# Kernel optimization log

Hardware: AMD Instinct MI355X
Metric: run time of the kernel (lower is better)

## Reference

```python
import jax, jax.numpy as jnp
import numpy as np

D_MODEL, N_LAYER, VOCAB = 166, 3, 26
D_INNER, D_STATE, D_CONV, DT_RANK = 332, 16, 4, 11
EPS = 1e-5


def setup_inputs() -> dict:
    key = jax.random.key(0)
    ks = jax.random.split(key, 12)
    B, L = 16, 1024
    n = lambda k, s, sc=0.05: jax.random.normal(k, s, jnp.float32) * sc
    # mamba-style dt bias init: softplus(bias) ~ U[1e-3, 0.1]
    dt_init = jax.random.uniform(ks[7], (N_LAYER, D_INNER), jnp.float32, 1e-3, 0.1)
    return {
        "fasta": jax.random.randint(ks[0], (B, L), 0, VOCAB),
        "embed": n(ks[1], (VOCAB, D_MODEL), 0.02),
        "in_proj_w": n(ks[2], (N_LAYER, 2 * D_INNER, D_MODEL)),
        "conv_w": n(ks[3], (N_LAYER, D_INNER, D_CONV), 0.2),
        "conv_b": n(ks[4], (N_LAYER, D_INNER), 0.02),
        "x_proj_w": n(ks[5], (N_LAYER, DT_RANK + 2 * D_STATE, D_INNER)),
        "dt_proj_w": n(ks[6], (N_LAYER, D_INNER, DT_RANK), 0.1),
        "dt_proj_b": jnp.log(jnp.expm1(dt_init)),
        "A_log": jnp.log(jnp.tile(jnp.arange(1, D_STATE + 1, dtype=jnp.float32), (N_LAYER, D_INNER, 1))),
        "D": jnp.ones((N_LAYER, D_INNER), jnp.float32),
        "out_proj_w": n(ks[8], (N_LAYER, D_MODEL, D_INNER)),
        "norm_w": jnp.ones((N_LAYER, D_MODEL), jnp.float32),
        "norm_f_w": jnp.ones((D_MODEL,), jnp.float32),
    }


def rmsnorm(x, w):
    return x * jax.lax.rsqrt(jnp.mean(x * x, axis=-1, keepdims=True) + EPS) * w


def mamba_layer(h, in_w, cw, cb, xw, dtw, dtb, A_log, Dp, ow):
    b, L, _ = h.shape
    xz = h @ in_w.T                              # (b, L, 2*d_inner)
    x, z = jnp.split(xz, 2, axis=-1)
    # causal depthwise conv1d, kernel D_CONV
    xp = jnp.pad(x, ((0, 0), (D_CONV - 1, 0), (0, 0)))
    x = sum(xp[:, j:j + L, :] * cw[:, j] for j in range(D_CONV)) + cb
    x = jax.nn.silu(x)                           # u: (b, L, d_inner)
    dbc = x @ xw.T                               # (b, L, dt_rank + 2*d_state)
    dt = dbc[..., :DT_RANK]
    Bm = dbc[..., DT_RANK:DT_RANK + D_STATE]
    Cm = dbc[..., DT_RANK + D_STATE:]
    dt = jax.nn.softplus(dt @ dtw.T + dtb)       # (b, L, d_inner)
    A = -jnp.exp(A_log)                          # (d_inner, d_state)
    # time-major selective scan
    ins = (jnp.moveaxis(dt, 1, 0), jnp.moveaxis(x, 1, 0),
           jnp.moveaxis(Bm, 1, 0), jnp.moveaxis(Cm, 1, 0))

    def step(hst, t):
        dt_i, x_i, B_i, C_i = t                  # (b,d) (b,d) (b,n) (b,n)
        dA = jnp.exp(dt_i[..., None] * A)        # (b, d, n)
        hst = dA * hst + (dt_i * x_i)[..., None] * B_i[:, None, :]
        y = jnp.einsum('bdn,bn->bd', hst, C_i)
        return hst, y

    h0 = jnp.zeros((b, D_INNER, D_STATE), x.dtype)
    _, ys = jax.lax.scan(step, h0, ins)
    y = jnp.moveaxis(ys, 0, 1) + Dp * x          # (b, L, d_inner)
    y = y * jax.nn.silu(z)
    return y @ ow.T                              # (b, L, d_model)


def reference(fasta, embed, in_proj_w, conv_w, conv_b, x_proj_w, dt_proj_w,
              dt_proj_b, A_log, D, out_proj_w, norm_w, norm_f_w):
    hidden = embed[fasta]                        # (b, L, d_model)
    residual = None
    for l in range(N_LAYER):
        residual = hidden if residual is None else hidden + residual
        hidden = rmsnorm(residual, norm_w[l])
        hidden = mamba_layer(hidden, in_proj_w[l], conv_w[l], conv_b[l],
                             x_proj_w[l], dt_proj_w[l], dt_proj_b[l],
                             A_log[l], D[l], out_proj_w[l])
    residual = hidden + residual
    v = rmsnorm(residual, norm_f_w)              # (b, L, d_model)
    ve = jnp.max(v, axis=1)                      # (b, d_model)
    return (ve, v)
```

## Files before the change

kernel.cpp:

```cpp
#include <hip/hip_runtime.h>
#include <math.h>

#define D_MODEL 166
#define N_LAYER 3
#define D_INNER 332
#define D_STATE 16
#define D_CONV  4
#define DT_RANK 11
#define BATCH   16
#define SEQ     1024
#define EPS     1e-5f
#define DBC_W   (DT_RANK + 2 * D_STATE)

#define CH 64
#define CL 16

#define KP_IN  192
#define KP_X   352

typedef unsigned short u16;
typedef __attribute__((ext_vector_type(8))) short short8;
typedef __attribute__((ext_vector_type(8))) unsigned short ushort8;
typedef __attribute__((ext_vector_type(4))) float f32x4;

__device__ inline u16 f2bf(float f) {
    unsigned int u = __float_as_uint(f);
    u += 0x7fff + ((u >> 16) & 1);
    return (u16)(u >> 16);
}
__device__ inline float bf2f(u16 u) {
    return __uint_as_float(((unsigned int)u) << 16);
}

__device__ inline void dt_step(float a, float& dtv, float& p) {
    if (a > 15.f) {
        dtv = a;
        p = __expf(-a);
    } else {
        float e = __expf(a);
        dtv = __logf(1.f + e);
        p = 1.f / (1.f + e);
    }
}

#define T1C (N_LAYER * 704 * KP_IN)
#define T2C (N_LAYER * 64 * KP_X)
#define T3C (N_LAYER * 192 * KP_X)
#define NB_CVT ((T1C + T2C + T3C + 255) / 256)
__global__ void k_prep(const int* __restrict__ fasta, const float* __restrict__ embed,
                       const float* __restrict__ w1, const float* __restrict__ w2,
                       const float* __restrict__ w3, const float* __restrict__ nw,
                       float* __restrict__ res, u16* __restrict__ o1,
                       u16* __restrict__ o2, u16* __restrict__ o3) {
    int blk = blockIdx.x;
    if (blk < BATCH * SEQ) {
        int m = threadIdx.x;
        if (m < D_MODEL)
            res[(size_t)blk * D_MODEL + m] = embed[(size_t)fasta[blk] * D_MODEL + m];
        return;
    }
    int idx = (blk - BATCH * SEQ) * 256 + threadIdx.x;
    if (idx < T1C) {
        int per = 704 * KP_IN;
        int l = idx / per, rr = idx - l * per;
        int n = rr / KP_IN, k = rr - n * KP_IN;
        float v = (n < 2 * D_INNER && k < D_MODEL)
                      ? w1[((size_t)l * 2 * D_INNER + n) * D_MODEL + k] * nw[l * D_MODEL + k]
                      : 0.f;
        o1[idx] = f2bf(v);
    } else if (idx < T1C + T2C) {
        int r = idx - T1C;
        int per = 64 * KP_X;
        int l = r / per, rr = r - l * per;
        int n = rr / KP_X, k = rr - n * KP_X;
        float v = (n < DBC_W && k < D_INNER) ? w2[((size_t)l * DBC_W + n) * D_INNER + k] : 0.f;
        o2[r] = f2bf(v);
    } else if (idx < T1C + T2C + T3C) {
        int r = idx - T1C - T2C;
        int per = 192 * KP_X;
        int l = r / per, rr = r - l * per;
        int n = rr / KP_X, k = rr - n * KP_X;
        float v = (n < D_MODEL && k < D_INNER) ? w3[((size_t)l * D_MODEL + n) * D_INNER + k] : 0.f;
        o3[r] = f2bf(v);
    }
}

__global__ __launch_bounds__(256) void k_gemm_in(const float* __restrict__ res,
                                                 const u16* __restrict__ Wbf,
                                                 u16* __restrict__ xb,
                                                 u16* __restrict__ zb) {
    __shared__ __align__(16) u16 As[128 * 40];
    __shared__ __align__(16) u16 Bs[64 * 40];
    __shared__ float sScale[128];
    int id = blockIdx.x;
    {
        int q = (int)gridDim.x >> 3;
        id = (id & 7) * q + (id >> 3);
    }
    int my = id / 11;
    int m0 = my * 128;
    int n0 = (id - my * 11) * 64;
    int t = threadIdx.x;
    int lr = t & 15, lk = (t >> 4) & 3;
    int wid = t >> 6, wr = wid & 1, wc = wid >> 1;
    int arow = t >> 2, ach = t & 3;

    f32x4 acc[4][2];
#pragma unroll
    for (int i = 0; i < 4; i++)
#pragma unroll
        for (int j = 0; j < 2; j++) acc[i][j] = (f32x4){0.f, 0.f, 0.f, 0.f};

    float ssq0 = 0.f, ssq1 = 0.f;
    for (int k0 = 0; k0 < KP_IN; k0 += 32) {
        int c0 = k0 + ach * 8;
#pragma unroll
        for (int half = 0; half < 2; half++) {
            int row = m0 + arow + half * 64;
            const float* rp = res + (size_t)row * D_MODEL;
            float v[8];
            if (c0 + 8 <= D_MODEL) {
#pragma unroll
                for (int j = 0; j < 4; j++) {
                    float2 f2 = *(const float2*)&rp[c0 + j * 2];
                    v[j * 2] = f2.x; v[j * 2 + 1] = f2.y;
                }
            } else {
#pragma unroll
                for (int j = 0; j < 8; j++) v[j] = (c0 + j < D_MODEL) ? rp[c0 + j] : 0.f;
            }
            float s = 0.f;
            ushort8 st;
#pragma unroll
            for (int j = 0; j < 8; j++) { s += v[j] * v[j]; st[j] = f2bf(v[j]); }
            if (half == 0) ssq0 += s; else ssq1 += s;
            *(ushort8*)&As[(arow + half * 64) * 40 + ach * 8] = st;
        }
        *(ushort8*)&Bs[arow * 40 + ach * 8] =
            *(const ushort8*)&Wbf[(size_t)(n0 + arow) * KP_IN + k0 + ach * 8];
        __syncthreads();
        short8 a[4], b[2];
#pragma unroll
        for (int mi = 0; mi < 4; mi++)
            a[mi] = *(const short8*)&As[(wr * 64 + mi * 16 + lr) * 40 + lk * 8];
#pragma unroll
        for (int ni = 0; ni < 2; ni++)
            b[ni] = *(const short8*)&Bs[(wc * 32 + ni * 16 + lr) * 40 + lk * 8];
#pragma unroll
        for (int mi = 0; mi < 4; mi++)
#pragma unroll
            for (int ni = 0; ni < 2; ni++)
                acc[mi][ni] = __builtin_amdgcn_mfma_f32_16x16x32_bf16(
                    a[mi], b[ni], acc[mi][ni], 0, 0, 0);
        __syncthreads();
    }
    ssq0 += __shfl_xor(ssq0, 1); ssq0 += __shfl_xor(ssq0, 2);
    ssq1 += __shfl_xor(ssq1, 1); ssq1 += __shfl_xor(ssq1, 2);
    if (ach == 0) {
        sScale[arow] = rsqrtf(ssq0 / (float)D_MODEL + EPS);
        sScale[arow + 64] = rsqrtf(ssq1 / (float)D_MODEL + EPS);
    }
    __syncthreads();

#pragma unroll
    for (int mi = 0; mi < 4; mi++) {
#pragma unroll
        for (int ni = 0; ni < 2; ni++) {
#pragma unroll
            for (int i = 0; i < 4; i++) {
                int rl = wr * 64 + mi * 16 + lk * 4 + i;
                int row = m0 + rl;
                int col = n0 + wc * 32 + ni * 16 + lr;
                float v = acc[mi][ni][i] * sScale[rl];
                if (col < D_INNER)
                    xb[(size_t)row * D_INNER + col] = f2bf(v);
                else if (col < 2 * D_INNER)
                    zb[(size_t)row * D_INNER + col - D_INNER] = f2bf(v);
            }
        }
    }
}

__global__ void k_conv(const u16* __restrict__ xb, const float* __restrict__ cw,
                       const float* __restrict__ cb, u16* __restrict__ xcb) {
    int bl = blockIdx.x;
    int pd = threadIdx.x;
    int d = pd * 2;
    unsigned int* outp = (unsigned int*)(xcb + (size_t)bl * KP_X);
    if (d < D_INNER) {
        int l = bl & (SEQ - 1);
        const unsigned int* p = (const unsigned int*)(xb + (size_t)bl * D_INNER) + pd;
        unsigned int v3 = p[0];
        unsigned int v2 = (l >= 1) ? p[-(D_INNER / 2)] : 0u;
        unsigned int v1 = (l >= 2) ? p[-2 * (D_INNER / 2)] : 0u;
        unsigned int v0 = (l >= 3) ? p[-3 * (D_INNER / 2)] : 0u;
        float4 wA = *(const float4*)&cw[d * 4];
        float4 wB = *(const float4*)&cw[(d + 1) * 4];
        float sa = cb[d]     + bf2f((u16)v0) * wA.x + bf2f((u16)v1) * wA.y +
                   bf2f((u16)v2) * wA.z + bf2f((u16)v3) * wA.w;
        float sb = cb[d + 1] + bf2f((u16)(v0 >> 16)) * wB.x + bf2f((u16)(v1 >> 16)) * wB.y +
                   bf2f((u16)(v2 >> 16)) * wB.z + bf2f((u16)(v3 >> 16)) * wB.w;
        float ra = sa / (1.f + __expf(-sa));
        float rb = sb / (1.f + __expf(-sb));
        outp[pd] = (unsigned int)f2bf(ra) | ((unsigned int)f2bf(rb) << 16);
    } else if (d < KP_X) {
        outp[pd] = 0u;
    }
}

__global__ __launch_bounds__(256) void k_gemm_x(const u16* __restrict__ Abf,
                                                const u16* __restrict__ Wbf,
                                                float* __restrict__ dbc) {
    __shared__ __align__(16) u16 As[64 * 40];
    __shared__ __align__(16) u16 Bs[64 * 40];
    int m0 = blockIdx.x * 64;
    int t = threadIdx.x;
    int lr = t & 15, lk = (t >> 4) & 3;
    int wid = t >> 6, wr = wid & 1, wc = wid >> 1;
    int arow = t >> 2, ach = t & 3;

    f32x4 acc[2][2];
#pragma unroll
    for (int i = 0; i < 2; i++)
#pragma unroll
        for (int j = 0; j < 2; j++) acc[i][j] = (f32x4){0.f, 0.f, 0.f, 0.f};

    for (int k0 = 0; k0 < KP_X; k0 += 32) {
        *(ushort8*)&As[arow * 40 + ach * 8] =
            *(const ushort8*)&Abf[(size_t)(m0 + arow) * KP_X + k0 + ach * 8];
        *(ushort8*)&Bs[arow * 40 + ach * 8] =
            *(const ushort8*)&Wbf[(size_t)arow * KP_X + k0 + ach * 8];
        __syncthreads();
        short8 a[2], b[2];
#pragma unroll
        for (int mi = 0; mi < 2; mi++)
            a[mi] = *(const short8*)&As[(wr * 32 + mi * 16 + lr) * 40 + lk * 8];
#pragma unroll
        for (int ni = 0; ni < 2; ni++)
            b[ni] = *(const short8*)&Bs[(wc * 32 + ni * 16 + lr) * 40 + lk * 8];
#pragma unroll
        for (int mi = 0; mi < 2; mi++)
#pragma unroll
            for (int ni = 0; ni < 2; ni++)
                acc[mi][ni] = __builtin_amdgcn_mfma_f32_16x16x32_bf16(
                    a[mi], b[ni], acc[mi][ni], 0, 0, 0);
        __syncthreads();
    }
#pragma unroll
    for (int mi = 0; mi < 2; mi++) {
#pragma unroll
        for (int ni = 0; ni < 2; ni++) {
#pragma unroll
            for (int i = 0; i < 4; i++) {
                int row = m0 + wr * 32 + mi * 16 + lk * 4 + i;
                int col = wc * 32 + ni * 16 + lr;
                if (col < DBC_W)
                    dbc[(size_t)row * DBC_W + col] = acc[mi][ni][i];
            }
        }
    }
}

__global__ __launch_bounds__(256) void k_gemm_out(const u16* __restrict__ Abf,
                                                  const u16* __restrict__ Wbf,
                                                  float* __restrict__ C) {
    __shared__ __align__(16) u16 As[128 * 40];
    __shared__ __align__(16) u16 Bs[64 * 40];
    int id = blockIdx.x;
    {
        int q = (int)gridDim.x >> 3;
        id = (id & 7) * q + (id >> 3);
    }
    int my = id / 3;
    int m0 = my * 128;
    int n0 = (id - my * 3) * 64;
    int t = threadIdx.x;
    int lr = t & 15, lk = (t >> 4) & 3;
    int wid = t >> 6, wr = wid & 1, wc = wid >> 1;
    int arow = t >> 2, ach = t & 3;

    f32x4 acc[4][2];
#pragma unroll
    for (int i = 0; i < 4; i++)
#pragma unroll
        for (int j = 0; j < 2; j++) acc[i][j] = (f32x4){0.f, 0.f, 0.f, 0.f};

    for (int k0 = 0; k0 < KP_X; k0 += 32) {
        *(ushort8*)&As[arow * 40 + ach * 8] =
            *(const ushort8*)&Abf[(size_t)(m0 + arow) * KP_X + k0 + ach * 8];
        *(ushort8*)&As[(arow + 64) * 40 + ach * 8] =
            *(const ushort8*)&Abf[(size_t)(m0 + arow + 64) * KP_X + k0 + ach * 8];
        *(ushort8*)&Bs[arow * 40 + ach * 8] =
            *(const ushort8*)&Wbf[(size_t)(n0 + arow) * KP_X + k0 + ach * 8];
        __syncthreads();
        short8 a[4], b[2];
#pragma unroll
        for (int mi = 0; mi < 4; mi++)
            a[mi] = *(const short8*)&As[(wr * 64 + mi * 16 + lr) * 40 + lk * 8];
#pragma unroll
        for (int ni = 0; ni < 2; ni++)
            b[ni] = *(const short8*)&Bs[(wc * 32 + ni * 16 + lr) * 40 + lk * 8];
#pragma unroll
        for (int mi = 0; mi < 4; mi++)
#pragma unroll
            for (int ni = 0; ni < 2; ni++)
                acc[mi][ni] = __builtin_amdgcn_mfma_f32_16x16x32_bf16(
                    a[mi], b[ni], acc[mi][ni], 0, 0, 0);
        __syncthreads();
    }
#pragma unroll
    for (int mi = 0; mi < 4; mi++) {
#pragma unroll
        for (int ni = 0; ni < 2; ni++) {
#pragma unroll
            for (int i = 0; i < 4; i++) {
                int row = m0 + wr * 64 + mi * 16 + lk * 4 + i;
                int col = n0 + wc * 32 + ni * 16 + lr;
                if (col < D_MODEL)
                    C[(size_t)row * D_MODEL + col] += acc[mi][ni][i];
            }
        }
    }
}

__global__ void k_scan1(const u16* __restrict__ xcb, const float* __restrict__ dbc,
                        const float* __restrict__ dtw, const float* __restrict__ dtb,
                        u16* __restrict__ h_end, float* __restrict__ pprod) {
    __shared__ float sD[CL][28];
    int b = blockIdx.x, c = blockIdx.y;
    int d = threadIdx.x;
    size_t base = (size_t)b * SEQ + (size_t)c * CL;
    for (int i = threadIdx.x; i < CL * 27; i += 384) {
        int tt = i / 27, cc = i - tt * 27;
        sD[tt][cc] = dbc[(base + tt) * DBC_W + cc];
    }
    __syncthreads();
    if (d >= D_INNER) return;
    float h[D_STATE];
#pragma unroll
    for (int n = 0; n < D_STATE; n++) h[n] = 0.f;
    float wr[DT_RANK];
#pragma unroll
    for (int r = 0; r < DT_RANK; r++) wr[r] = dtw[(size_t)d * DT_RANK + r];
    float bias = dtb[d];
    float Pacc = 1.f;
#pragma unroll 4
    for (int tt = 0; tt < CL; tt++) {
        size_t idx = base + tt;
        float xv = bf2f(xcb[idx * KP_X + d]);
        float a = bias;
#pragma unroll
        for (int r = 0; r < DT_RANK; r++) a += sD[tt][r] * wr[r];
        float dtv, p;
        dt_step(a, dtv, p);
        Pacc *= p;
        float bx = dtv * xv;
        float pw = p;
#pragma unroll
        for (int n = 0; n < D_STATE; n++) {
            h[n] = pw * h[n] + bx * sD[tt][11 + n];
            pw *= p;
        }
    }
    size_t hb = (((size_t)b * CH + c) * D_INNER + d) * D_STATE;
    ushort8 st0, st1;
#pragma unroll
    for (int n = 0; n < 8; n++) { st0[n] = f2bf(h[n]); st1[n] = f2bf(h[n + 8]); }
    *(ushort8*)&h_end[hb] = st0;
    *(ushort8*)&h_end[hb + 8] = st1;
    pprod[((size_t)b * CH + c) * D_INNER + d] = Pacc;
}

__global__ void k_scan2(const float* __restrict__ pprod, u16* __restrict__ h_end) {
    int b = blockIdx.x;
    int i = blockIdx.y * 128 + threadIdx.x;
    if (i >= D_INNER * D_STATE) return;
    int d = i >> 4, n = i & 15;
    int e = n + 1;
    size_t pb = (size_t)b * CH * D_INNER + d;
    float q = pprod[pb];
    float tmp = bf2f(h_end[pb * D_STATE + n]);
    float h = 0.f;
    for (int c = 0; c < CH; c++) {
        size_t cur = pb + (size_t)c * D_INNER;
        size_t nxt = (c + 1 < CH) ? cur + D_INNER : cur;
        float qn = pprod[nxt];
        float tn = bf2f(h_end[nxt * D_STATE + n]);
        float pw = 1.f, bb = q;
        int ee = e;
#pragma unroll
        for (int s = 0; s < 5; s++) {
            if (ee & 1) pw *= bb;
            bb *= bb;
            ee >>= 1;
        }
        h_end[cur * D_STATE + n] = f2bf(h);
        h = pw * h + tmp;
        q = qn; tmp = tn;
    }
}

__global__ void k_scan3(const u16* __restrict__ xcb, const u16* __restrict__ zb,
                        const float* __restrict__ dbc,
                        const float* __restrict__ dtw, const float* __restrict__ dtb,
                        const float* __restrict__ Dp, const u16* __restrict__ h_start,
                        u16* __restrict__ ybf) {
    __shared__ float sD[CL][44];
    int b = blockIdx.x, c = blockIdx.y;
    int d = threadIdx.x;
    size_t base = (size_t)b * SEQ + (size_t)c * CL;
    for (int i = threadIdx.x; i < CL * DBC_W; i += 384) {
        int tt = i / DBC_W, cc = i - tt * DBC_W;
        sD[tt][cc] = dbc[(base + tt) * DBC_W + cc];
    }
    __syncthreads();
    if (d >= D_INNER) {
        if (d < KP_X)
            for (int tt = 0; tt < CL; tt++) ybf[(base + tt) * KP_X + d] = 0;
        return;
    }
    float h[D_STATE];
    size_t hb = (((size_t)b * CH + c) * D_INNER + d) * D_STATE;
    ushort8 ld0 = *(const ushort8*)&h_start[hb];
    ushort8 ld1 = *(const ushort8*)&h_start[hb + 8];
#pragma unroll
    for (int n = 0; n < 8; n++) { h[n] = bf2f(ld0[n]); h[n + 8] = bf2f(ld1[n]); }
    float wr[DT_RANK];
#pragma unroll
    for (int r = 0; r < DT_RANK; r++) wr[r] = dtw[(size_t)d * DT_RANK + r];
    float bias = dtb[d];
    float Dd = Dp[d];
#pragma unroll 4
    for (int tt = 0; tt < CL; tt++) {
        size_t idx = base + tt;
        float xv = bf2f(xcb[idx * KP_X + d]);
        float zv = bf2f(zb[idx * D_INNER + d]);
        float a = bias;
#pragma unroll
        for (int r = 0; r < DT_RANK; r++) a += sD[tt][r] * wr[r];
        float dtv, p;
        dt_step(a, dtv, p);
        float bx = dtv * xv;
        float yv = 0.f;
        float pw = p;
#pragma unroll
        for (int n = 0; n < D_STATE; n++) {
            h[n] = pw * h[n] + bx * sD[tt][11 + n];
            yv += h[n] * sD[tt][27 + n];
            pw *= p;
        }
        yv += Dd * xv;
        float sig = 1.f / (1.f + __expf(-zv));
        ybf[idx * KP_X + d] = f2bf(yv * (zv * sig));
    }
}

__global__ __launch_bounds__(256) void k_finalnorm(const float* __restrict__ res,
                                                   const float* __restrict__ w,
                                                   float* __restrict__ v_out,
                                                   float* __restrict__ pmax) {
    __shared__ float tile[32][167];
    __shared__ float sc[32];
    int b = blockIdx.x, c = blockIdx.y;
    int t = threadIdx.x;
    size_t r0 = (size_t)b * SEQ + c * 32;
    for (int i = t; i < 32 * D_MODEL; i += 256) {
        int row = i / D_MODEL, m = i - row * D_MODEL;
        tile[row][m] = res[(r0 + row) * D_MODEL + m];
    }
    __syncthreads();
    if (t < 32) {
        float s = 0.f;
        for (int m = 0; m < D_MODEL; m++) { float v = tile[t][m]; s += v * v; }
        sc[t] = rsqrtf(s / (float)D_MODEL + EPS);
    }
    __syncthreads();
    for (int i = t; i < 32 * D_MODEL; i += 256) {
        int row = i / D_MODEL, m = i - row * D_MODEL;
        v_out[(r0 + row) * D_MODEL + m] = tile[row][m] * sc[row] * w[m];
    }
    if (t < D_MODEL) {
        float wv = w[t];
        float mx = -1e30f;
        for (int row = 0; row < 32; row++)
            mx = fmaxf(mx, tile[row][t] * sc[row] * wv);
        pmax[((size_t)b * 32 + c) * D_MODEL + t] = mx;
    }
}

__global__ void k_fmax(const float* __restrict__ pmax, float* __restrict__ ve) {
    int b = blockIdx.x;
    int m = threadIdx.x;
    if (m >= D_MODEL) return;
    float mx = -1e30f;
    for (int c = 0; c < 32; c++) mx = fmaxf(mx, pmax[((size_t)b * 32 + c) * D_MODEL + m]);
    ve[(size_t)b * D_MODEL + m] = mx;
}

extern "C" void kernel_launch(void* const* d_in, const int* in_sizes, int n_in,
                              void* d_out, int out_size, void* d_ws, size_t ws_size,
                              hipStream_t stream) {
    const int* fasta = (const int*)d_in[0];
    const float* embed = (const float*)d_in[1];
    const float* in_proj_w = (const float*)d_in[2];
    const float* conv_w = (const float*)d_in[3];
    const float* conv_b = (const float*)d_in[4];
    const float* x_proj_w = (const float*)d_in[5];
    const float* dt_proj_w = (const float*)d_in[6];
    const float* dt_proj_b = (const float*)d_in[7];
    const float* Dp = (const float*)d_in[9];
    const float* out_proj_w = (const float*)d_in[10];
    const float* norm_w = (const float*)d_in[11];
    const float* norm_f_w = (const float*)d_in[12];

    const size_t BL = (size_t)BATCH * SEQ;
    float* ws = (float*)d_ws;
    float* res   = ws;
    float* dbc   = res + BL * D_MODEL;
    float* pprod = dbc + BL * DBC_W;
    float* pmax  = pprod + (size_t)BATCH * CH * D_INNER;
    float* fend  = pmax + BATCH * 32 * D_MODEL;
    u16* xb    = (u16*)fend;
    u16* zb    = xb + BL * D_INNER;
    u16* xcb   = zb + BL * D_INNER;
    u16* ybf   = xcb + BL * KP_X;
    u16* h_end = ybf + BL * KP_X;
    u16* w_in  = h_end + (size_t)BATCH * CH * D_INNER * D_STATE;
    u16* w_x   = w_in + (size_t)T1C;
    u16* w_out = w_x + (size_t)T2C;

    float* ve_out = (float*)d_out;
    float* v_out = ve_out + BATCH * D_MODEL;

    k_prep<<<(int)BL + NB_CVT, 256, 0, stream>>>(
        fasta, embed, in_proj_w, x_proj_w, out_proj_w, norm_w, res, w_in, w_x, w_out);

    for (int l = 0; l < N_LAYER; l++) {
        const float* dtwl = dt_proj_w + (size_t)l * D_INNER * DT_RANK;
        const float* dtbl = dt_proj_b + (size_t)l * D_INNER;

        k_gemm_in<<<128 * 11, 256, 0, stream>>>(
            res, w_in + (size_t)l * 704 * KP_IN, xb, zb);
        k_conv<<<BL, 192, 0, stream>>>(
            xb, conv_w + (size_t)l * D_INNER * D_CONV, conv_b + (size_t)l * D_INNER, xcb);
        k_gemm_x<<<256, 256, 0, stream>>>(
            xcb, w_x + (size_t)l * 64 * KP_X, dbc);
        k_scan1<<<dim3(16, CH), 384, 0, stream>>>(
            xcb, dbc, dtwl, dtbl, h_end, pprod);
        k_scan2<<<dim3(16, 42), 128, 0, stream>>>(pprod, h_end);
        k_scan3<<<dim3(16, CH), 384, 0, stream>>>(
            xcb, zb, dbc, dtwl, dtbl, Dp + (size_t)l * D_INNER, h_end, ybf);
        k_gemm_out<<<128 * 3, 256, 0, stream>>>(
            ybf, w_out + (size_t)l * 192 * KP_X, res);
    }

    k_finalnorm<<<dim3(16, 32), 256, 0, stream>>>(res, norm_f_w, v_out, pmax);
    k_fmax<<<16, 192, 0, stream>>>(pmax, ve_out);
}
```

Baseline: 466.1 us.

## Fuse causal conv+SiLU into in-projection GEMM epilogue and merge final max reduction

The depthwise causal conv and SiLU are now computed in the k_gemm_in epilogue from an LDS tile of the x outputs. The three halo rows before each 128-row tile are recomputed with a scalar dot product over the bf16 weights. This removes the separate k_conv launch and the xb round trip through global memory. The final max reduction is folded into k_finalnorm with a last-block-done atomic counter, removing the k_fmax launch. The halo recomputation adds serial scalar work to the x-tile blocks, and the pad zeroing plus counter reset move into k_prep.

```diff
diff --git a/kernel.cpp b/kernel.cpp
--- a/kernel.cpp
+++ b/kernel.cpp
@@ -51,12 +51,16 @@
                        const float* __restrict__ w1, const float* __restrict__ w2,
                        const float* __restrict__ w3, const float* __restrict__ nw,
                        float* __restrict__ res, u16* __restrict__ o1,
-                       u16* __restrict__ o2, u16* __restrict__ o3) {
+                       u16* __restrict__ o2, u16* __restrict__ o3,
+                       u16* __restrict__ xcb, unsigned int* __restrict__ ctrs) {
     int blk = blockIdx.x;
     if (blk < BATCH * SEQ) {
         int m = threadIdx.x;
         if (m < D_MODEL)
             res[(size_t)blk * D_MODEL + m] = embed[(size_t)fasta[blk] * D_MODEL + m];
+        else if (m >= 166 && m < 176)
+            ((unsigned int*)xcb)[(size_t)blk * (KP_X / 2) + 166 + (m - 166)] = 0u;
+        if (m == 200 && blk < BATCH) ctrs[blk] = 0u;
         return;
     }
     int idx = (blk - BATCH * SEQ) * 256 + threadIdx.x;
@@ -87,11 +91,14 @@
 
 __global__ __launch_bounds__(256) void k_gemm_in(const float* __restrict__ res,
                                                  const u16* __restrict__ Wbf,
-                                                 u16* __restrict__ xb,
+                                                 const float* __restrict__ cw,
+                                                 const float* __restrict__ cb,
+                                                 u16* __restrict__ xcb,
                                                  u16* __restrict__ zb) {
-    __shared__ __align__(16) u16 As[128 * 40];
-    __shared__ __align__(16) u16 Bs[64 * 40];
+    __shared__ __align__(16) u16 pool[131 * 64];
     __shared__ float sScale[128];
+    u16* As = pool;
+    u16* Bs = pool + 128 * 40;
     int id = blockIdx.x;
     {
         int q = (int)gridDim.x >> 3;
@@ -162,6 +169,7 @@
     }
     __syncthreads();
 
+    bool xtile = (n0 < D_INNER);
 #pragma unroll
     for (int mi = 0; mi < 4; mi++) {
 #pragma unroll
@@ -173,38 +181,48 @@
                 int col = n0 + wc * 32 + ni * 16 + lr;
                 float v = acc[mi][ni][i] * sScale[rl];
                 if (col < D_INNER)
-                    xb[(size_t)row * D_INNER + col] = f2bf(v);
+                    pool[(rl + 3) * 64 + (col - n0)] = f2bf(v);
                 else if (col < 2 * D_INNER)
                     zb[(size_t)row * D_INNER + col - D_INNER] = f2bf(v);
             }
         }
     }
-}
-
-__global__ void k_conv(const u16* __restrict__ xb, const float* __restrict__ cw,
-                       const float* __restrict__ cb, u16* __restrict__ xcb) {
-    int bl = blockIdx.x;
-    int pd = threadIdx.x;
-    int d = pd * 2;
-    unsigned int* outp = (unsigned int*)(xcb + (size_t)bl * KP_X);
-    if (d < D_INNER) {
-        int l = bl & (SEQ - 1);
-        const unsigned int* p = (const unsigned int*)(xb + (size_t)bl * D_INNER) + pd;
-        unsigned int v3 = p[0];
-        unsigned int v2 = (l >= 1) ? p[-(D_INNER / 2)] : 0u;
-        unsigned int v1 = (l >= 2) ? p[-2 * (D_INNER / 2)] : 0u;
-        unsigned int v0 = (l >= 3) ? p[-3 * (D_INNER / 2)] : 0u;
-        float4 wA = *(const float4*)&cw[d * 4];
-        float4 wB = *(const float4*)&cw[(d + 1) * 4];
-        float sa = cb[d]     + bf2f((u16)v0) * wA.x + bf2f((u16)v1) * wA.y +
-                   bf2f((u16)v2) * wA.z + bf2f((u16)v3) * wA.w;
-        float sb = cb[d + 1] + bf2f((u16)(v0 >> 16)) * wB.x + bf2f((u16)(v1 >> 16)) * wB.y +
-                   bf2f((u16)(v2 >> 16)) * wB.z + bf2f((u16)(v3 >> 16)) * wB.w;
-        float ra = sa / (1.f + __expf(-sa));
-        float rb = sb / (1.f + __expf(-sb));
-        outp[pd] = (unsigned int)f2bf(ra) | ((unsigned int)f2bf(rb) << 16);
-    } else if (d < KP_X) {
-        outp[pd] = 0u;
+    if (xtile && (m0 & (SEQ - 1)) != 0 && t < 192) {
+        int br = t >> 6, lane = t & 63;
+        int gr = m0 - 3 + br;
+        const float* rp = res + (size_t)gr * D_MODEL;
+        float s = 0.f;
+        for (int k = lane; k < D_MODEL; k += 64) { float v = rp[k]; s += v * v; }
+#pragma unroll
+        for (int o = 32; o; o >>= 1) s += __shfl_xor(s, o);
+        float scale = rsqrtf(s / (float)D_MODEL + EPS);
+        int col = n0 + lane;
+        if (col < D_INNER) {
+            float dot = 0.f;
+            for (int k = 0; k < D_MODEL; k++)
+                dot += bf2f(f2bf(rp[k])) * bf2f(Wbf[(size_t)col * KP_IN + k]);
+            pool[br * 64 + lane] = f2bf(dot * scale);
+        }
+    }
+    __syncthreads();
+    if (xtile) {
+        int ncx = (D_INNER - n0 < 64) ? (D_INNER - n0) : 64;
+        for (int i = t; i < 128 * 64; i += 256) {
+            int row = i >> 6, col = i & 63;
+            if (col < ncx) {
+                int gr = m0 + row;
+                int l = gr & (SEQ - 1);
+                int d = n0 + col;
+                float4 w4 = *(const float4*)&cw[d * 4];
+                float s = cb[d];
+                if (l >= 3) s += bf2f(pool[(row + 0) * 64 + col]) * w4.x;
+                if (l >= 2) s += bf2f(pool[(row + 1) * 64 + col]) * w4.y;
+                if (l >= 1) s += bf2f(pool[(row + 2) * 64 + col]) * w4.z;
+                s += bf2f(pool[(row + 3) * 64 + col]) * w4.w;
+                float sig = 1.f / (1.f + __expf(-s));
+                xcb[(size_t)gr * KP_X + d] = f2bf(s * sig);
+            }
+        }
     }
 }
 
@@ -458,9 +476,12 @@
 __global__ __launch_bounds__(256) void k_finalnorm(const float* __restrict__ res,
                                                    const float* __restrict__ w,
                                                    float* __restrict__ v_out,
-                                                   float* __restrict__ pmax) {
+                                                   unsigned int* __restrict__ pmaxu,
+                                                   unsigned int* __restrict__ cnt,
+                                                   float* __restrict__ ve) {
     __shared__ float tile[32][167];
     __shared__ float sc[32];
+    __shared__ int sLast;
     int b = blockIdx.x, c = blockIdx.y;
     int t = threadIdx.x;
     size_t r0 = (size_t)b * SEQ + c * 32;
@@ -484,17 +505,26 @@
         float mx = -1e30f;
         for (int row = 0; row < 32; row++)
             mx = fmaxf(mx, tile[row][t] * sc[row] * wv);
-        pmax[((size_t)b * 32 + c) * D_MODEL + t] = mx;
-    }
-}
-
-__global__ void k_fmax(const float* __restrict__ pmax, float* __restrict__ ve) {
-    int b = blockIdx.x;
-    int m = threadIdx.x;
-    if (m >= D_MODEL) return;
-    float mx = -1e30f;
-    for (int c = 0; c < 32; c++) mx = fmaxf(mx, pmax[((size_t)b * 32 + c) * D_MODEL + m]);
-    ve[(size_t)b * D_MODEL + m] = mx;
+        __hip_atomic_store(&pmaxu[((size_t)b * 32 + c) * D_MODEL + t],
+                           __float_as_uint(mx), __ATOMIC_RELAXED,
+                           __HIP_MEMORY_SCOPE_AGENT);
+    }
+    __syncthreads();
+    if (t == 0) {
+        unsigned int old = __hip_atomic_fetch_add(&cnt[b], 1u, __ATOMIC_ACQ_REL,
+                                                  __HIP_MEMORY_SCOPE_AGENT);
+        sLast = (old == 31);
+    }
+    __syncthreads();
+    if (sLast && t < D_MODEL) {
+        float mx = -1e30f;
+        for (int c2 = 0; c2 < 32; c2++) {
+            unsigned int u = __hip_atomic_load(&pmaxu[((size_t)b * 32 + c2) * D_MODEL + t],
+                                               __ATOMIC_RELAXED, __HIP_MEMORY_SCOPE_AGENT);
+            mx = fmaxf(mx, __uint_as_float(u));
+        }
+        ve[(size_t)b * D_MODEL + t] = mx;
+    }
 }
 
 extern "C" void kernel_launch(void* const* d_in, const int* in_sizes, int n_in,
@@ -518,10 +548,9 @@
     float* res   = ws;
     float* dbc   = res + BL * D_MODEL;
     float* pprod = dbc + BL * DBC_W;
-    float* pmax  = pprod + (size_t)BATCH * CH * D_INNER;
-    float* fend  = pmax + BATCH * 32 * D_MODEL;
-    u16* xb    = (u16*)fend;
-    u16* zb    = xb + BL * D_INNER;
+    unsigned int* pmaxu = (unsigned int*)(pprod + (size_t)BATCH * CH * D_INNER);
+    unsigned int* ctrs  = pmaxu + BATCH * 32 * D_MODEL;
+    u16* zb    = (u16*)(ctrs + BATCH);
     u16* xcb   = zb + BL * D_INNER;
     u16* ybf   = xcb + BL * KP_X;
     u16* h_end = ybf + BL * KP_X;
@@ -533,16 +562,17 @@
     float* v_out = ve_out + BATCH * D_MODEL;
 
     k_prep<<<(int)BL + NB_CVT, 256, 0, stream>>>(
-        fasta, embed, in_proj_w, x_proj_w, out_proj_w, norm_w, res, w_in, w_x, w_out);
+        fasta, embed, in_proj_w, x_proj_w, out_proj_w, norm_w, res, w_in, w_x, w_out,
+        xcb, ctrs);
 
     for (int l = 0; l < N_LAYER; l++) {
         const float* dtwl = dt_proj_w + (size_t)l * D_INNER * DT_RANK;
         const float* dtbl = dt_proj_b + (size_t)l * D_INNER;
 
         k_gemm_in<<<128 * 11, 256, 0, stream>>>(
-            res, w_in + (size_t)l * 704 * KP_IN, xb, zb);
-        k_conv<<<BL, 192, 0, stream>>>(
-            xb, conv_w + (size_t)l * D_INNER * D_CONV, conv_b + (size_t)l * D_INNER, xcb);
+            res, w_in + (size_t)l * 704 * KP_IN,
+            conv_w + (size_t)l * D_INNER * D_CONV, conv_b + (size_t)l * D_INNER,
+            xcb, zb);
         k_gemm_x<<<256, 256, 0, stream>>>(
             xcb, w_x + (size_t)l * 64 * KP_X, dbc);
         k_scan1<<<dim3(16, CH), 384, 0, stream>>>(
@@ -554,6 +584,6 @@
             ybf, w_out + (size_t)l * 192 * KP_X, res);
     }
 
-    k_finalnorm<<<dim3(16, 32), 256, 0, stream>>>(res, norm_f_w, v_out, pmax);
-    k_fmax<<<16, 192, 0, stream>>>(pmax, ve_out);
-}
+    k_finalnorm<<<dim3(16, 32), 256, 0, stream>>>(res, norm_f_w, v_out, pmaxu, ctrs,
+                                                  ve_out);
+}
```

Measured after the change: 594.0 us. 1.27x slower.
